# Kernel optimization log

Measured on AMD Instinct MI355X. Metric: run time of the kernel, lower is better.

## Reference

```python
import jax, jax.numpy as jnp
import numpy as np

BLOCKSIZE = 128
NUM_EXPERTS = 16
TOP_K = 6
HIDDEN = 2048
INTER = 1408
TOKENS = 4096
N_BLK_H = HIDDEN // BLOCKSIZE   # 16
N_BLK_I = -(-INTER // BLOCKSIZE)  # 11 (ceil)


def setup_inputs() -> dict:
    key = jax.random.key(0)
    ks = jax.random.split(key, 8)
    x = jax.random.normal(ks[0], (TOKENS, HIDDEN), dtype=jnp.float32)
    selected_experts = jax.random.randint(ks[1], (TOKENS, TOP_K), 0, NUM_EXPERTS)
    # quantized-style weights + per-block scales (dequant = w * repeat(s, blocksize))
    w0 = jax.random.normal(ks[2], (NUM_EXPERTS, INTER, HIDDEN), dtype=jnp.float32) * 0.02
    s0 = jax.random.uniform(ks[3], (NUM_EXPERTS, INTER, N_BLK_H), dtype=jnp.float32, minval=0.5, maxval=1.5)
    w1 = jax.random.normal(ks[4], (NUM_EXPERTS, INTER, HIDDEN), dtype=jnp.float32) * 0.02
    s1 = jax.random.uniform(ks[5], (NUM_EXPERTS, INTER, N_BLK_H), dtype=jnp.float32, minval=0.5, maxval=1.5)
    w2 = jax.random.normal(ks[6], (NUM_EXPERTS, HIDDEN, INTER), dtype=jnp.float32) * 0.02
    s2 = jax.random.uniform(ks[7], (NUM_EXPERTS, HIDDEN, N_BLK_I), dtype=jnp.float32, minval=0.5, maxval=1.5)
    return {"x": x, "selected_experts": selected_experts,
            "w0": w0, "s0": s0, "w1": w1, "s1": s1, "w2": w2, "s2": s2}


def _dequant(w, s):
    # w: [E, O, I], s: [E, O, ceil(I/bs)] -> broadcast each scale over its block
    s_full = jnp.repeat(s, BLOCKSIZE, axis=-1)[..., : w.shape[-1]]
    return w * s_full


def reference(x, selected_experts, w0, s0, w1, s1, w2, s2):
    # Dequantize block-quantized expert weights.
    W0 = _dequant(w0, s0)  # gate proj [E, I, H]
    W1 = _dequant(w1, s1)  # up proj   [E, I, H]
    W2 = _dequant(w2, s2)  # down proj [E, H, I]
    # Original loops token x slot, calling expert(x[i]). Equivalent batched form:
    # compute every expert on every token, then gather by (token, slot) index.
    gate = jnp.einsum('th,eih->eti', x, W0)            # [E, T, I]
    up = jnp.einsum('th,eih->eti', x, W1)              # [E, T, I]
    act = jax.nn.silu(gate) * up                       # [E, T, I]
    all_out = jnp.einsum('eti,ehi->eth', act, W2)      # [E, T, H]
    tok = jnp.arange(x.shape[0])[:, None]              # [T, 1]
    out = all_out[selected_experts, tok]               # [T, K, H]
    return out
```

## Files before the change

kernel.cpp:

```cpp
#include <hip/hip_runtime.h>
#include <stdint.h>

#define TOKENS 4096
#define HIDDEN 2048
#define INTER  1408
#define NEXP   16
#define TOPK   6
#define NPAIR  (TOKENS*TOPK)
#define BM     128
#define MAXTILES (NPAIR/BM + NEXP)
#define MAXT2  (NPAIR/256 + NEXP)
#define NT1    (INTER/128)
#define NT2    (HIDDEN/128)

typedef __attribute__((ext_vector_type(8))) short bf16x8;
typedef __attribute__((ext_vector_type(4))) float f32x4;

__device__ __forceinline__ short f2bf(float f){
  union { float f; uint32_t u; } v; v.f = f;
  uint32_t r = (v.u + 0x7FFFu + ((v.u >> 16) & 1u)) >> 16;
  return (short)(r & 0xFFFFu);
}

__device__ __forceinline__ void gld16(const void* g, const void* l){
  __builtin_amdgcn_global_load_lds((const __attribute__((address_space(1))) void*)g,
                                   (__attribute__((address_space(3))) void*)l, 16, 0, 0);
}

#define SB() __builtin_amdgcn_sched_barrier(0)
#define BAR() __builtin_amdgcn_s_barrier()
#define WAITV(n) asm volatile("s_waitcnt vmcnt(" #n ")" ::: "memory")
#define WAITL() asm volatile("s_waitcnt lgkmcnt(0)" ::: "memory")


__global__ void k_xcast(const float* __restrict__ x, short* __restrict__ xb){
  int i = (blockIdx.x * 256 + threadIdx.x) * 8;
  f32x4 a = *(const f32x4*)(x + i);
  f32x4 b = *(const f32x4*)(x + i + 4);
  bf16x8 o;
  #pragma unroll
  for (int j = 0; j < 4; ++j){ o[j] = f2bf(a[j]); o[4+j] = f2bf(b[j]); }
  *(bf16x8*)(xb + i) = o;
}

__global__ void k_dequant(const float* __restrict__ w, const float* __restrict__ s,
                          short* __restrict__ o, int rowlen, int nblk){
  const int row = blockIdx.x;
  const size_t base = (size_t)row * rowlen;
  for (int c = threadIdx.x * 8; c < rowlen; c += blockDim.x * 8){
    float sc = s[(size_t)row * nblk + (c >> 7)];
    f32x4 a = *(const f32x4*)(w + base + c);
    f32x4 b = *(const f32x4*)(w + base + c + 4);
    bf16x8 h;
    #pragma unroll
    for (int j = 0; j < 4; ++j){ h[j] = f2bf(a[j] * sc); h[4+j] = f2bf(b[j] * sc); }
    *(bf16x8*)(o + base + c) = h;
  }
}

__global__ void k_count(const int* __restrict__ sel, int* __restrict__ cnt){
  int p = blockIdx.x * 256 + threadIdx.x;
  if (p < NPAIR) atomicAdd(&cnt[sel[p]], 1);
}

__global__ void k_scan(const int* __restrict__ cnt, int* __restrict__ offsets,
                       int2* __restrict__ tiles, int* __restrict__ ntiles,
                       int2* __restrict__ tiles2, int* __restrict__ ntiles2){
  if (threadIdx.x != 0) return;
  int off = 0, nt = 0, nt2 = 0;
  for (int e = 0; e < NEXP; ++e){
    offsets[e] = off;
    int c = cnt[e];
    for (int m = 0; m < c; m += BM){
      int rows = c - m; if (rows > BM) rows = BM;
      tiles[nt++] = make_int2(off + m, (e << 16) | rows);
    }
    for (int m = 0; m < c; m += 256){
      int rows = c - m; if (rows > 256) rows = 256;
      tiles2[nt2++] = make_int2(off + m, (e << 16) | rows);
    }
    off += c;
  }
  offsets[NEXP] = off;
  *ntiles = nt;
  *ntiles2 = nt2;
}

__global__ void k_scatter(const int* __restrict__ sel, const int* __restrict__ offsets,
                          int* __restrict__ cursor, int* __restrict__ pair_tk){
  int p = blockIdx.x * 256 + threadIdx.x;
  if (p >= NPAIR) return;
  int e = sel[p];
  int pos = offsets[e] + atomicAdd(&cursor[e], 1);
  pair_tk[pos] = (p / TOPK) * 8 + (p % TOPK);
}


__global__ __launch_bounds__(512) void k_g1(
    const short* __restrict__ xb,
    const short* __restrict__ w0b, const short* __restrict__ w1b,
    const int2* __restrict__ tiles2, const int* __restrict__ ntiles2,
    const int* __restrict__ pair_tk, short* __restrict__ act)
{
  const int nwg = MAXT2 * NT1;
  const int orig = (int)(blockIdx.y * MAXT2 + blockIdx.x);
  const int wg = (orig & 7) * (nwg >> 3) + (orig >> 3);
  const int tx = wg % MAXT2, ty = wg / MAXT2;
  if (tx >= *ntiles2) return;
  const int2 td = tiles2[tx];
  const int mstart = td.x;
  const int e  = td.y >> 16;
  const int vr = td.y & 0xFFFF;

  __shared__ short lA[4][8192];
  __shared__ short lB[4][8192];

  const int tid = threadIdx.x, w = tid >> 6, lane = tid & 63;

  const short* pA[2]; const short* pB[2]; int sg8[2];
  #pragma unroll
  for (int i = 0; i < 2; ++i){
    int s = (w * 2 + i) * 64 + lane;
    int r = s >> 2, j = (s & 3) ^ ((s >> 3) & 3);
    sg8[i] = s * 8;
    int p = mstart + r; if (p >= NPAIR) p = NPAIR - 1;
    pA[i] = xb + (size_t)(pair_tk[p] >> 3) * HIDDEN + j * 8;
    int G = r >> 4, srow = (G >> 1) * 16 + (r & 15);
    const short* wsrc = (G & 1) ? w1b : w0b;
    pB[i] = wsrc + ((size_t)e * INTER + (size_t)ty * 128 + srow) * HIDDEN + j * 8;
  }
  auto stage = [&](int slot, int ko){
    #pragma unroll
    for (int i = 0; i < 2; ++i) gld16(pA[i] + ko, &lA[slot][sg8[i]]);
    #pragma unroll
    for (int i = 0; i < 2; ++i) gld16(pB[i] + ko, &lB[slot][sg8[i]]);
  };

  f32x4 acc[4][8];
  #pragma unroll
  for (int i = 0; i < 4; ++i)
    #pragma unroll
    for (int j = 0; j < 8; ++j) acc[i][j] = (f32x4)0.f;

  const int cc = lane & 15, ks = lane >> 4;
  const int sx = (ks ^ ((cc >> 1) & 3)) * 8;
  const int wm = w >> 1, wn = w & 1;
  int arow[4], brow[8];
  #pragma unroll
  for (int mf = 0; mf < 4; ++mf) arow[mf] = (wm * 64 + mf * 16 + cc) * 32;
  #pragma unroll
  for (int nf = 0; nf < 8; ++nf) brow[nf] = (wn * 128 + nf * 16 + cc) * 32;

  stage(0, 0); stage(1, 32); stage(2, 64); stage(3, 96);

  #pragma unroll 1
  for (int t = 0; t < 32; ++t){
    const int b = t & 1;
    if (t == 0)      { WAITV(12); }
    else if (t < 31) { WAITV(8);  }
    else             { WAITV(4);  }
    SB(); BAR(); SB();
    {
      bf16x8 a0[4], bb[8];
      #pragma unroll
      for (int mf = 0; mf < 4; ++mf) a0[mf] = *(const bf16x8*)&lA[b*2][arow[mf] + sx];
      #pragma unroll
      for (int nf = 0; nf < 8; ++nf) bb[nf] = *(const bf16x8*)&lB[b*2][brow[nf] + sx];
      if (t >= 1 && t + 1 < 32) stage(((t+1)&1)*2 + 1, (t+1)*64 + 32);
      WAITL(); SB();
      __builtin_amdgcn_s_setprio(1);
      #pragma unroll
      for (int nf = 0; nf < 8; ++nf)
        #pragma unroll
        for (int mf = 0; mf < 4; ++mf)
          acc[mf][nf] = __builtin_amdgcn_mfma_f32_16x16x32_bf16(a0[mf], bb[nf], acc[mf][nf], 0, 0, 0);
      __builtin_amdgcn_s_setprio(0);
      SB(); BAR(); SB();
    }
    if (t < 31) { WAITV(8); } else { WAITV(0); }
    SB(); BAR(); SB();
    {
      bf16x8 a0[4], bb[8];
      #pragma unroll
      for (int mf = 0; mf < 4; ++mf) a0[mf] = *(const bf16x8*)&lA[b*2+1][arow[mf] + sx];
      #pragma unroll
      for (int nf = 0; nf < 8; ++nf) bb[nf] = *(const bf16x8*)&lB[b*2+1][brow[nf] + sx];
      if (t + 2 < 32) stage(b*2, (t+2)*64);
      WAITL(); SB();
      __builtin_amdgcn_s_setprio(1);
      #pragma unroll
      for (int nf = 0; nf < 8; ++nf)
        #pragma unroll
        for (int mf = 0; mf < 4; ++mf)
          acc[mf][nf] = __builtin_amdgcn_mfma_f32_16x16x32_bf16(a0[mf], bb[nf], acc[mf][nf], 0, 0, 0);
      __builtin_amdgcn_s_setprio(0);
      SB(); BAR(); SB();
    }
  }

  #pragma unroll
  for (int mf = 0; mf < 4; ++mf){
    #pragma unroll
    for (int j = 0; j < 4; ++j){
      int row = wm * 64 + mf * 16 + ks * 4 + j;
      if (row < vr){
        short* ar = act + (size_t)(mstart + row) * INTER + (size_t)ty * 128 + cc;
        #pragma unroll
        for (int q = 0; q < 4; ++q){
          float g = acc[mf][2*q][j], u = acc[mf][2*q+1][j];
          float a = g / (1.f + __expf(-g)) * u;
          ar[(wn * 4 + q) * 16] = f2bf(a);
        }
      }
    }
  }
}

__global__ __launch_bounds__(512) void k_g2(
    const short* __restrict__ act, const short* __restrict__ w2b,
    const int2* __restrict__ tiles2, const int* __restrict__ ntiles2,
    const int* __restrict__ pair_tk, float* __restrict__ out)
{
  const int nwg = MAXT2 * NT2;
  const int orig = (int)(blockIdx.y * MAXT2 + blockIdx.x);
  const int wg = (orig & 7) * (nwg >> 3) + (orig >> 3);
  const int tx = wg % MAXT2, ty = wg / MAXT2;
  if (tx >= *ntiles2) return;
  const int2 td = tiles2[tx];
  const int mstart = td.x;
  const int e  = td.y >> 16;
  const int vr = td.y & 0xFFFF;

  __shared__ short lA[4][8192];
  __shared__ short lB[4][4096];

  const int tid = threadIdx.x, w = tid >> 6, lane = tid & 63;

  const short* pA[2]; int sg8[2];
  #pragma unroll
  for (int i = 0; i < 2; ++i){
    int s = (w * 2 + i) * 64 + lane;
    int r = s >> 2, j = (s & 3) ^ ((s >> 3) & 3);
    sg8[i] = s * 8;
    int p = mstart + r; if (p >= NPAIR) p = NPAIR - 1;
    pA[i] = act + (size_t)p * INTER + j * 8;
  }
  const short* pB; int sb8;
  {
    int s = tid;
    int r = s >> 2, j = (s & 3) ^ ((s >> 3) & 3);
    sb8 = s * 8;
    pB = w2b + ((size_t)e * HIDDEN + (size_t)ty * 128 + r) * INTER + j * 8;
  }
  auto stage = [&](int slot, int ko){
    #pragma unroll
    for (int i = 0; i < 2; ++i) gld16(pA[i] + ko, &lA[slot][sg8[i]]);
    gld16(pB + ko, &lB[slot][sb8]);
  };

  f32x4 acc[4][4];
  #pragma unroll
  for (int i = 0; i < 4; ++i)
    #pragma unroll
    for (int j = 0; j < 4; ++j) acc[i][j] = (f32x4)0.f;

  const int cc = lane & 15, ks = lane >> 4;
  const int sx = (ks ^ ((cc >> 1) & 3)) * 8;
  const int wm = w >> 1, wn = w & 1;
  int arow[4], brow[4];
  #pragma unroll
  for (int mf = 0; mf < 4; ++mf) arow[mf] = (wm * 64 + mf * 16 + cc) * 32;
  #pragma unroll
  for (int nf = 0; nf < 4; ++nf) brow[nf] = (wn * 64 + nf * 16 + cc) * 32;

  stage(0, 0); stage(1, 32); stage(2, 64); stage(3, 96);

  #pragma unroll 1
  for (int t = 0; t < 22; ++t){
    const int b = t & 1;
    if (t == 0)      { WAITV(9); }
    else if (t < 21) { WAITV(6); }
    else             { WAITV(3); }
    SB(); BAR(); SB();
    {
      bf16x8 a0[4], bb[4];
      #pragma unroll
      for (int mf = 0; mf < 4; ++mf) a0[mf] = *(const bf16x8*)&lA[b*2][arow[mf] + sx];
      #pragma unroll
      for (int nf = 0; nf < 4; ++nf) bb[nf] = *(const bf16x8*)&lB[b*2][brow[nf] + sx];
      if (t >= 1 && t + 1 < 22) stage(((t+1)&1)*2 + 1, (t+1)*64 + 32);
      WAITL(); SB();
      __builtin_amdgcn_s_setprio(1);
      #pragma unroll
      for (int nf = 0; nf < 4; ++nf)
        #pragma unroll
        for (int mf = 0; mf < 4; ++mf)
          acc[mf][nf] = __builtin_amdgcn_mfma_f32_16x16x32_bf16(a0[mf], bb[nf], acc[mf][nf], 0, 0, 0);
      __builtin_amdgcn_s_setprio(0);
      SB(); BAR(); SB();
    }
    if (t < 21) { WAITV(6); } else { WAITV(0); }
    SB(); BAR(); SB();
    {
      bf16x8 a0[4], bb[4];
      #pragma unroll
      for (int mf = 0; mf < 4; ++mf) a0[mf] = *(const bf16x8*)&lA[b*2+1][arow[mf] + sx];
      #pragma unroll
      for (int nf = 0; nf < 4; ++nf) bb[nf] = *(const bf16x8*)&lB[b*2+1][brow[nf] + sx];
      if (t + 2 < 22) stage(b*2, (t+2)*64);
      WAITL(); SB();
      __builtin_amdgcn_s_setprio(1);
      #pragma unroll
      for (int nf = 0; nf < 4; ++nf)
        #pragma unroll
        for (int mf = 0; mf < 4; ++mf)
          acc[mf][nf] = __builtin_amdgcn_mfma_f32_16x16x32_bf16(a0[mf], bb[nf], acc[mf][nf], 0, 0, 0);
      __builtin_amdgcn_s_setprio(0);
      SB(); BAR(); SB();
    }
  }

  #pragma unroll
  for (int mf = 0; mf < 4; ++mf){
    #pragma unroll
    for (int j = 0; j < 4; ++j){
      int row = wm * 64 + mf * 16 + ks * 4 + j;
      if (row < vr){
        int ptk = pair_tk[mstart + row];
        float* orow = out + ((size_t)(ptk >> 3) * TOPK + (ptk & 7)) * HIDDEN
                      + (size_t)ty * 128 + wn * 64 + cc;
        #pragma unroll
        for (int nf = 0; nf < 4; ++nf)
          orow[nf * 16] = acc[mf][nf][j];
      }
    }
  }
}


__global__ __launch_bounds__(256) void k_gemm1(
    const short* __restrict__ xb,
    const float* __restrict__ w0, const float* __restrict__ s0,
    const float* __restrict__ w1, const float* __restrict__ s1,
    const int2* __restrict__ tiles, const int* __restrict__ ntiles,
    const int* __restrict__ pair_tk, short* __restrict__ act)
{
  if ((int)blockIdx.x >= *ntiles) return;
  const int2 td = tiles[blockIdx.x];
  const int mstart = td.x;
  const int e  = td.y >> 16;
  const int vr = td.y & 0xFFFF;
  const int tid = threadIdx.x;
  const int lane = tid & 63;

  __shared__ short lA[BM * 32];
  __shared__ short lB0[BM * 40];
  __shared__ short lB1[BM * 40];

  const int r0 = tid >> 2, r1 = 64 + (tid >> 2);
  const int seg = tid & 3;
  int p0 = mstart + r0; if (p0 >= NPAIR) p0 = NPAIR - 1;
  int p1 = mstart + r1; if (p1 >= NPAIR) p1 = NPAIR - 1;
  const short* arow0 = xb + (size_t)(pair_tk[p0] >> 3) * HIDDEN + (seg ^ ((r0 >> 1) & 3)) * 8;
  const short* arow1 = xb + (size_t)(pair_tk[p1] >> 3) * HIDDEN + (seg ^ ((r1 >> 1) & 3)) * 8;
  const short* ldsA0 = &lA[tid * 8];
  const short* ldsA1 = &lA[2048 + tid * 8];

  const int brow = tid >> 1, half = tid & 1;
  const int gbrow = blockIdx.y * BM + brow;
  const float* w0row = w0 + ((size_t)e * INTER + gbrow) * HIDDEN + half * 16;
  const float* w1row = w1 + ((size_t)e * INTER + gbrow) * HIDDEN + half * 16;
  const float* s0row = s0 + ((size_t)e * INTER + gbrow) * (HIDDEN / 128);
  const float* s1row = s1 + ((size_t)e * INTER + gbrow) * (HIDDEN / 128);
  short* lb0w = &lB0[brow * 40 + half * 16];
  short* lb1w = &lB1[brow * 40 + half * 16];

  f32x4 acc0[4][4], acc1[4][4];
  #pragma unroll
  for (int i = 0; i < 4; ++i)
    #pragma unroll
    for (int j = 0; j < 4; ++j){ acc0[i][j] = (f32x4)0.f; acc1[i][j] = (f32x4)0.f; }

  const int wm = tid >> 7, wn = (tid >> 6) & 1;
  const int cc = lane & 15, ks = lane >> 4;

  for (int kt = 0; kt < HIDDEN / 32; ++kt){
    gld16(arow0 + kt * 32, ldsA0);
    gld16(arow1 + kt * 32, ldsA1);
    {
      float sc = s0row[kt >> 2];
      const float* g = w0row + kt * 32;
      f32x4 q0 = *(const f32x4*)g,       q1 = *(const f32x4*)(g + 4),
            q2 = *(const f32x4*)(g + 8), q3 = *(const f32x4*)(g + 12);
      bf16x8 h0, h1;
      #pragma unroll
      for (int i = 0; i < 4; ++i){
        h0[i] = f2bf(q0[i] * sc); h0[4 + i] = f2bf(q1[i] * sc);
        h1[i] = f2bf(q2[i] * sc); h1[4 + i] = f2bf(q3[i] * sc);
      }
      *(bf16x8*)lb0w = h0; *(bf16x8*)(lb0w + 8) = h1;
    }
    {
      float sc = s1row[kt >> 2];
      const float* g = w1row + kt * 32;
      f32x4 q0 = *(const f32x4*)g,       q1 = *(const f32x4*)(g + 4),
            q2 = *(const f32x4*)(g + 8), q3 = *(const f32x4*)(g + 12);
      bf16x8 h0, h1;
      #pragma unroll
      for (int i = 0; i < 4; ++i){
        h0[i] = f2bf(q0[i] * sc); h0[4 + i] = f2bf(q1[i] * sc);
        h1[i] = f2bf(q2[i] * sc); h1[4 + i] = f2bf(q3[i] * sc);
      }
      *(bf16x8*)lb1w = h0; *(bf16x8*)(lb1w + 8) = h1;
    }
    __syncthreads();

    bf16x8 af[4];
    #pragma unroll
    for (int mf = 0; mf < 4; ++mf){
      int row = wm * 64 + mf * 16 + cc;
      af[mf] = *(const bf16x8*)&lA[row * 32 + ((ks ^ ((row >> 1) & 3)) * 8)];
    }
    #pragma unroll
    for (int nf = 0; nf < 4; ++nf){
      int rb = wn * 64 + nf * 16 + cc;
      bf16x8 b0 = *(const bf16x8*)&lB0[rb * 40 + ks * 8];
      bf16x8 b1 = *(const bf16x8*)&lB1[rb * 40 + ks * 8];
      #pragma unroll
      for (int mf = 0; mf < 4; ++mf)
        acc0[mf][nf] = __builtin_amdgcn_mfma_f32_16x16x32_bf16(af[mf], b0, acc0[mf][nf], 0, 0, 0);
      #pragma unroll
      for (int mf = 0; mf < 4; ++mf)
        acc1[mf][nf] = __builtin_amdgcn_mfma_f32_16x16x32_bf16(af[mf], b1, acc1[mf][nf], 0, 0, 0);
    }
    __syncthreads();
  }

  const int rbase = wm * 64 + (lane >> 4) * 4;
  #pragma unroll
  for (int mf = 0; mf < 4; ++mf){
    #pragma unroll
    for (int j = 0; j < 4; ++j){
      int row = rbase + mf * 16 + j;
      if (row < vr){
        short* ar = act + (size_t)(mstart + row) * INTER + blockIdx.y * BM + wn * 64 + cc;
        #pragma unroll
        for (int nf = 0; nf < 4; ++nf){
          float g = acc0[mf][nf][j], u = acc1[mf][nf][j];
          float a = g / (1.f + __expf(-g)) * u;
          ar[nf * 16] = f2bf(a);
        }
      }
    }
  }
}

__global__ __launch_bounds__(256) void k_gemm2(
    const short* __restrict__ act,
    const float* __restrict__ w2, const float* __restrict__ s2,
    const int2* __restrict__ tiles, const int* __restrict__ ntiles,
    const int* __restrict__ pair_tk, float* __restrict__ out)
{
  if ((int)blockIdx.x >= *ntiles) return;
  const int2 td = tiles[blockIdx.x];
  const int mstart = td.x;
  const int e  = td.y >> 16;
  const int vr = td.y & 0xFFFF;
  const int tid = threadIdx.x;
  const int lane = tid & 63;

  __shared__ short lA[BM * 32];
  __shared__ short lB[BM * 40];

  const int r0 = tid >> 2, r1 = 64 + (tid >> 2);
  const int seg = tid & 3;
  int p0 = mstart + r0; if (p0 >= NPAIR) p0 = NPAIR - 1;
  int p1 = mstart + r1; if (p1 >= NPAIR) p1 = NPAIR - 1;
  const short* arow0 = act + (size_t)p0 * INTER + (seg ^ ((r0 >> 1) & 3)) * 8;
  const short* arow1 = act + (size_t)p1 * INTER + (seg ^ ((r1 >> 1) & 3)) * 8;
  const short* ldsA0 = &lA[tid * 8];
  const short* ldsA1 = &lA[2048 + tid * 8];

  const int brow = tid >> 1, half = tid & 1;
  const int gbrow = blockIdx.y * BM + brow;
  const float* w2row = w2 + ((size_t)e * HIDDEN + gbrow) * INTER + half * 16;
  const float* s2row = s2 + ((size_t)e * HIDDEN + gbrow) * 11;
  short* lbw = &lB[brow * 40 + half * 16];

  f32x4 acc[4][4];
  #pragma unroll
  for (int i = 0; i < 4; ++i)
    #pragma unroll
    for (int j = 0; j < 4; ++j) acc[i][j] = (f32x4)0.f;

  const int wm = tid >> 7, wn = (tid >> 6) & 1;
  const int cc = lane & 15, ks = lane >> 4;

  for (int kt = 0; kt < INTER / 32; ++kt){
    gld16(arow0 + kt * 32, ldsA0);
    gld16(arow1 + kt * 32, ldsA1);
    {
      float sc = s2row[kt >> 2];
      const float* g = w2row + kt * 32;
      f32x4 q0 = *(const f32x4*)g,       q1 = *(const f32x4*)(g + 4),
            q2 = *(const f32x4*)(g + 8), q3 = *(const f32x4*)(g + 12);
      bf16x8 h0, h1;
      #pragma unroll
      for (int i = 0; i < 4; ++i){
        h0[i] = f2bf(q0[i] * sc); h0[4 + i] = f2bf(q1[i] * sc);
        h1[i] = f2bf(q2[i] * sc); h1[4 + i] = f2bf(q3[i] * sc);
      }
      *(bf16x8*)lbw = h0; *(bf16x8*)(lbw + 8) = h1;
    }
    __syncthreads();

    bf16x8 af[4];
    #pragma unroll
    for (int mf = 0; mf < 4; ++mf){
      int row = wm * 64 + mf * 16 + cc;
      af[mf] = *(const bf16x8*)&lA[row * 32 + ((ks ^ ((row >> 1) & 3)) * 8)];
    }
    #pragma unroll
    for (int nf = 0; nf < 4; ++nf){
      int rb = wn * 64 + nf * 16 + cc;
      bf16x8 b = *(const bf16x8*)&lB[rb * 40 + ks * 8];
      #pragma unroll
      for (int mf = 0; mf < 4; ++mf)
        acc[mf][nf] = __builtin_amdgcn_mfma_f32_16x16x32_bf16(af[mf], b, acc[mf][nf], 0, 0, 0);
    }
    __syncthreads();
  }

  const int rbase = wm * 64 + (lane >> 4) * 4;
  #pragma unroll
  for (int mf = 0; mf < 4; ++mf){
    #pragma unroll
    for (int j = 0; j < 4; ++j){
      int row = rbase + mf * 16 + j;
      if (row < vr){
        int ptk = pair_tk[mstart + row];
        float* orow = out + ((size_t)(ptk >> 3) * TOPK + (ptk & 7)) * HIDDEN
                      + blockIdx.y * BM + wn * 64 + cc;
        #pragma unroll
        for (int nf = 0; nf < 4; ++nf)
          orow[nf * 16] = acc[mf][nf][j];
      }
    }
  }
}


extern "C" void kernel_launch(void* const* d_in, const int* in_sizes, int n_in,
                              void* d_out, int out_size, void* d_ws, size_t ws_size,
                              hipStream_t stream)
{
  const float* x  = (const float*)d_in[0];
  const int*   sel= (const int*)  d_in[1];
  const float* w0 = (const float*)d_in[2];
  const float* s0 = (const float*)d_in[3];
  const float* w1 = (const float*)d_in[4];
  const float* s1 = (const float*)d_in[5];
  const float* w2 = (const float*)d_in[6];
  const float* s2 = (const float*)d_in[7];
  float* out = (float*)d_out;

  char* ws = (char*)d_ws;
  size_t o = 0;
  auto alloc = [&](size_t n){ size_t r = o; o = (o + n + 255) & ~(size_t)255; return r; };
  int*  cnt     = (int*) (ws + alloc(64));
  int*  cursor  = (int*) (ws + alloc(64));
  int*  offsets = (int*) (ws + alloc(68));
  int*  ntiles  = (int*) (ws + alloc(4));
  int*  ntiles2 = (int*) (ws + alloc(4));
  int2* tiles   = (int2*)(ws + alloc(MAXTILES * 8));
  int2* tiles2  = (int2*)(ws + alloc(MAXT2 * 8));
  int*  pair_tk = (int*) (ws + alloc((size_t)NPAIR * 4));
  short* xb     = (short*)(ws + alloc((size_t)TOKENS * HIDDEN * 2));
  short* act    = (short*)(ws + alloc((size_t)NPAIR * INTER * 2));
  const size_t WSZ = (size_t)NEXP * INTER * HIDDEN * 2;
  short* w0b    = (short*)(ws + alloc(WSZ));
  short* w1b    = (short*)(ws + alloc(WSZ));
  short* w2b    = (short*)(ws + alloc(WSZ));
  const bool predeq = (ws_size >= o);
  (void)in_sizes; (void)n_in; (void)out_size;

  hipMemsetAsync(ws, 0, 512, stream);

  k_xcast  <<<(TOKENS * HIDDEN) / (256 * 8), 256, 0, stream>>>(x, xb);
  k_count  <<<(NPAIR + 255) / 256, 256, 0, stream>>>(sel, cnt);
  k_scan   <<<1, 64, 0, stream>>>(cnt, offsets, tiles, ntiles, tiles2, ntiles2);
  k_scatter<<<(NPAIR + 255) / 256, 256, 0, stream>>>(sel, offsets, cursor, pair_tk);

  if (predeq){
    k_dequant<<<NEXP * INTER,  256, 0, stream>>>(w0, s0, w0b, HIDDEN, HIDDEN / 128);
    k_dequant<<<NEXP * INTER,  256, 0, stream>>>(w1, s1, w1b, HIDDEN, HIDDEN / 128);
    k_g1<<<dim3(MAXT2, NT1), 512, 0, stream>>>(xb, w0b, w1b,
                                               tiles2, ntiles2, pair_tk, act);
    k_dequant<<<NEXP * HIDDEN, 256, 0, stream>>>(w2, s2, w2b, INTER, 11);
    k_g2<<<dim3(MAXT2, NT2), 512, 0, stream>>>(act, w2b,
                                               tiles2, ntiles2, pair_tk, out);
  } else {
    k_gemm1<<<dim3(MAXTILES, NT1), 256, 0, stream>>>(xb, w0, s0, w1, s1,
                                                     tiles, ntiles, pair_tk, act);
    k_gemm2<<<dim3(MAXTILES, NT2), 256, 0, stream>>>(act, w2, s2,
                                                     tiles, ntiles, pair_tk, out);
  }
}
```

Baseline: 922.3 us.

## Widen down-proj GEMM tile to 256 columns and fuse/streamline dequant kernels

```diff
diff --git a/kernel.cpp b/kernel.cpp
--- a/kernel.cpp
+++ b/kernel.cpp
@@ -12,6 +12,7 @@
 #define MAXT2  (NPAIR/256 + NEXP)
 #define NT1    (INTER/128)
 #define NT2    (HIDDEN/128)
+#define NT2W   (HIDDEN/256)
 
 typedef __attribute__((ext_vector_type(8))) short bf16x8;
 typedef __attribute__((ext_vector_type(4))) float f32x4;
@@ -27,6 +28,10 @@
                                    (__attribute__((address_space(3))) void*)l, 16, 0, 0);
 }
 
+__device__ __forceinline__ f32x4 ntld4(const float* p){
+  return __builtin_nontemporal_load((const f32x4*)p);
+}
+
 #define SB() __builtin_amdgcn_sched_barrier(0)
 #define BAR() __builtin_amdgcn_s_barrier()
 #define WAITV(n) asm volatile("s_waitcnt vmcnt(" #n ")" ::: "memory")
@@ -35,12 +40,47 @@
 
 __global__ void k_xcast(const float* __restrict__ x, short* __restrict__ xb){
   int i = (blockIdx.x * 256 + threadIdx.x) * 8;
-  f32x4 a = *(const f32x4*)(x + i);
-  f32x4 b = *(const f32x4*)(x + i + 4);
+  f32x4 a = ntld4(x + i);
+  f32x4 b = ntld4(x + i + 4);
   bf16x8 o;
   #pragma unroll
   for (int j = 0; j < 4; ++j){ o[j] = f2bf(a[j]); o[4+j] = f2bf(b[j]); }
   *(bf16x8*)(xb + i) = o;
+}
+
+__global__ void k_deq01(const float* __restrict__ w0, const float* __restrict__ s0,
+                        const float* __restrict__ w1, const float* __restrict__ s1,
+                        short* __restrict__ o0, short* __restrict__ o1){
+  int row = blockIdx.x;
+  const float* w; const float* s; short* o;
+  if (row < NEXP * INTER){ w = w0; s = s0; o = o0; }
+  else { row -= NEXP * INTER; w = w1; s = s1; o = o1; }
+  const size_t base = (size_t)row * HIDDEN;
+  const int c = threadIdx.x * 8;
+  float sc = s[(size_t)row * (HIDDEN/128) + (c >> 7)];
+  f32x4 a = ntld4(w + base + c);
+  f32x4 b = ntld4(w + base + c + 4);
+  bf16x8 h;
+  #pragma unroll
+  for (int j = 0; j < 4; ++j){ h[j] = f2bf(a[j] * sc); h[4+j] = f2bf(b[j] * sc); }
+  *(bf16x8*)(o + base + c) = h;
+}
+
+__global__ void k_deqw2(const float* __restrict__ w2, const float* __restrict__ s2,
+                        short* __restrict__ o){
+  const int total = NEXP * HIDDEN * (INTER / 8);
+  for (int gi = blockIdx.x * 256 + threadIdx.x; gi < total; gi += gridDim.x * 256){
+    int row = gi / (INTER / 8);
+    int c = (gi - row * (INTER / 8)) * 8;
+    const size_t base = (size_t)row * INTER;
+    float sc = s2[(size_t)row * 11 + (c >> 7)];
+    f32x4 a = ntld4(w2 + base + c);
+    f32x4 b = ntld4(w2 + base + c + 4);
+    bf16x8 h;
+    #pragma unroll
+    for (int j = 0; j < 4; ++j){ h[j] = f2bf(a[j] * sc); h[4+j] = f2bf(b[j] * sc); }
+    *(bf16x8*)(o + base + c) = h;
+  }
 }
 
 __global__ void k_dequant(const float* __restrict__ w, const float* __restrict__ s,
@@ -221,7 +261,7 @@
     const int2* __restrict__ tiles2, const int* __restrict__ ntiles2,
     const int* __restrict__ pair_tk, float* __restrict__ out)
 {
-  const int nwg = MAXT2 * NT2;
+  const int nwg = MAXT2 * NT2W;
   const int orig = (int)(blockIdx.y * MAXT2 + blockIdx.x);
   const int wg = (orig & 7) * (nwg >> 3) + (orig >> 3);
   const int tx = wg % MAXT2, ty = wg / MAXT2;
@@ -232,11 +272,11 @@
   const int vr = td.y & 0xFFFF;
 
   __shared__ short lA[4][8192];
-  __shared__ short lB[4][4096];
+  __shared__ short lB[4][8192];
 
   const int tid = threadIdx.x, w = tid >> 6, lane = tid & 63;
 
-  const short* pA[2]; int sg8[2];
+  const short* pA[2]; const short* pB[2]; int sg8[2];
   #pragma unroll
   for (int i = 0; i < 2; ++i){
     int s = (w * 2 + i) * 64 + lane;
@@ -244,74 +284,69 @@
     sg8[i] = s * 8;
     int p = mstart + r; if (p >= NPAIR) p = NPAIR - 1;
     pA[i] = act + (size_t)p * INTER + j * 8;
-  }
-  const short* pB; int sb8;
-  {
-    int s = tid;
-    int r = s >> 2, j = (s & 3) ^ ((s >> 3) & 3);
-    sb8 = s * 8;
-    pB = w2b + ((size_t)e * HIDDEN + (size_t)ty * 128 + r) * INTER + j * 8;
+    pB[i] = w2b + ((size_t)e * HIDDEN + (size_t)ty * 256 + r) * INTER + j * 8;
   }
   auto stage = [&](int slot, int ko){
     #pragma unroll
     for (int i = 0; i < 2; ++i) gld16(pA[i] + ko, &lA[slot][sg8[i]]);
-    gld16(pB + ko, &lB[slot][sb8]);
+    #pragma unroll
+    for (int i = 0; i < 2; ++i) gld16(pB[i] + ko, &lB[slot][sg8[i]]);
   };
 
-  f32x4 acc[4][4];
+  f32x4 acc[4][8];
   #pragma unroll
   for (int i = 0; i < 4; ++i)
     #pragma unroll
-    for (int j = 0; j < 4; ++j) acc[i][j] = (f32x4)0.f;
+    for (int j = 0; j < 8; ++j) acc[i][j] = (f32x4)0.f;
 
   const int cc = lane & 15, ks = lane >> 4;
   const int sx = (ks ^ ((cc >> 1) & 3)) * 8;
   const int wm = w >> 1, wn = w & 1;
-  int arow[4], brow[4];
+  int arow[4], brow[8];
   #pragma unroll
   for (int mf = 0; mf < 4; ++mf) arow[mf] = (wm * 64 + mf * 16 + cc) * 32;
   #pragma unroll
-  for (int nf = 0; nf < 4; ++nf) brow[nf] = (wn * 64 + nf * 16 + cc) * 32;
+  for (int nf = 0; nf < 8; ++nf) brow[nf] = (wn * 128 + nf * 16 + cc) * 32;
 
   stage(0, 0); stage(1, 32); stage(2, 64); stage(3, 96);
 
   #pragma unroll 1
   for (int t = 0; t < 22; ++t){
     const int b = t & 1;
-    if (t == 0)      { WAITV(9); }
-    else if (t < 21) { WAITV(6); }
-    else             { WAITV(3); }
+    if (t == 0)      { WAITV(12); }
+    else if (t < 21) { WAITV(8);  }
+    else             { WAITV(4);  }
     SB(); BAR(); SB();
     {
-      bf16x8 a0[4], bb[4];
+      bf16x8 a0[4], bb[8];
       #pragma unroll
       for (int mf = 0; mf < 4; ++mf) a0[mf] = *(const bf16x8*)&lA[b*2][arow[mf] + sx];
       #pragma unroll
-      for (int nf = 0; nf < 4; ++nf) bb[nf] = *(const bf16x8*)&lB[b*2][brow[nf] + sx];
+      for (int nf = 0; nf < 8; ++nf) bb[nf] = *(const bf16x8*)&lB[b*2][brow[nf] + sx];
       if (t >= 1 && t + 1 < 22) stage(((t+1)&1)*2 + 1, (t+1)*64 + 32);
       WAITL(); SB();
       __builtin_amdgcn_s_setprio(1);
       #pragma unroll
-      for (int nf = 0; nf < 4; ++nf)
+      for (int nf = 0; nf < 8; ++nf)
         #pragma unroll
         for (int mf = 0; mf < 4; ++mf)
           acc[mf][nf] = __builtin_amdgcn_mfma_f32_16x16x32_bf16(a0[mf], bb[nf], acc[mf][nf], 0, 0, 0);
       __builtin_amdgcn_s_setprio(0);
       SB(); BAR(); SB();
     }
-    if (t < 21) { WAITV(6); } else { WAITV(0); }
+    if (t < 21) { WAITV(8); } else { WAITV(0); }
     SB(); BAR(); SB();
     {
-      bf16x8 a0[4], bb[4];
+      bf16x8 a0[4], bb[8];
       #pragma unroll
       for (int mf = 0; mf < 4; ++mf) a0[mf] = *(const bf16x8*)&lA[b*2+1][arow[mf] + sx];
       #pragma unroll
-      for (int nf = 0; nf < 4; ++nf) bb[nf] = *(const bf16x8*)&lB[b*2+1][brow[nf] + sx];
+      for (int nf = 0; nf < 8; ++nf) bb[nf] = *(const bf16x8*)&lB[b*2+1][brow[nf] + sx];
       if (t + 2 < 22) stage(b*2, (t+2)*64);
       WAITL(); SB();
       __builtin_amdgcn_s_setprio(1);
       #pragma unroll
-      for (int nf = 0; nf < 4; ++nf)
+      for (int nf = 0; nf < 8; ++nf)
         #pragma unroll
         for (int mf = 0; mf < 4; ++mf)
           acc[mf][nf] = __builtin_amdgcn_mfma_f32_16x16x32_bf16(a0[mf], bb[nf], acc[mf][nf], 0, 0, 0);
@@ -328,9 +363,9 @@
       if (row < vr){
         int ptk = pair_tk[mstart + row];
         float* orow = out + ((size_t)(ptk >> 3) * TOPK + (ptk & 7)) * HIDDEN
-                      + (size_t)ty * 128 + wn * 64 + cc;
-        #pragma unroll
-        for (int nf = 0; nf < 4; ++nf)
+                      + (size_t)ty * 256 + wn * 128 + cc;
+        #pragma unroll
+        for (int nf = 0; nf < 8; ++nf)
           orow[nf * 16] = acc[mf][nf][j];
       }
     }
@@ -592,13 +627,12 @@
   k_scatter<<<(NPAIR + 255) / 256, 256, 0, stream>>>(sel, offsets, cursor, pair_tk);
 
   if (predeq){
-    k_dequant<<<NEXP * INTER,  256, 0, stream>>>(w0, s0, w0b, HIDDEN, HIDDEN / 128);
-    k_dequant<<<NEXP * INTER,  256, 0, stream>>>(w1, s1, w1b, HIDDEN, HIDDEN / 128);
+    k_deq01<<<2 * NEXP * INTER, 256, 0, stream>>>(w0, s0, w1, s1, w0b, w1b);
     k_g1<<<dim3(MAXT2, NT1), 512, 0, stream>>>(xb, w0b, w1b,
                                                tiles2, ntiles2, pair_tk, act);
-    k_dequant<<<NEXP * HIDDEN, 256, 0, stream>>>(w2, s2, w2b, INTER, 11);
-    k_g2<<<dim3(MAXT2, NT2), 512, 0, stream>>>(act, w2b,
-                                               tiles2, ntiles2, pair_tk, out);
+    k_deqw2<<<2048, 256, 0, stream>>>(w2, s2, w2b);
+    k_g2<<<dim3(MAXT2, NT2W), 512, 0, stream>>>(act, w2b,
+                                                tiles2, ntiles2, pair_tk, out);
   } else {
     k_gemm1<<<dim3(MAXTILES, NT1), 256, 0, stream>>>(xb, w0, s0, w1, s1,
                                                      tiles, ntiles, pair_tk, act);
```

New measurement: 818.4 us. -11.3%, faster.
